# Kernel tuning notes

Hardware: AMD Instinct MI355X
Metric: run time of the kernel (lower is better)

## Reference

```python
import jax, jax.numpy as jnp
import numpy as np


def setup_inputs() -> dict:
    key = jax.random.key(0)
    k_x, k_w1, k_w2 = jax.random.split(key, 3)
    b, d, m, h = 256, 2048, 64, 128  # batch, d_model, history_length, d_out
    lim1 = 1.0 / np.sqrt(m + h)
    lim2 = 1.0 / np.sqrt(h + d)
    x = jax.random.normal(k_x, (b, d, m), dtype=jnp.float32)
    w1 = jax.random.uniform(k_w1, (m, h, d), dtype=jnp.float32, minval=-lim1, maxval=lim1)
    b1 = jnp.zeros((1, h, d), dtype=jnp.float32)
    w2 = jax.random.uniform(k_w2, (h, d), dtype=jnp.float32, minval=-lim2, maxval=lim2)
    b2 = jnp.zeros((1, h), dtype=jnp.float32)
    return {"x": x, "w1": w1, "b1": b1, "w2": w2, "b2": b2}


def reference(x, w1, b1, w2, b2):
    # per-neuron (per-d) MLP: contract over history m, then over hidden h
    hidden = jnp.einsum('bdm,mhd->bhd', x, w1) + b1  # (b, h, d)
    out = jnp.einsum('bhd,hd->bh', hidden, w2) + b2  # (b, h)
    return out
```

## Files before the change

### kernel.cpp

```cpp
#include <hip/hip_runtime.h>

typedef unsigned short u16;
typedef __attribute__((ext_vector_type(8))) short short8;
typedef __attribute__((ext_vector_type(4))) float f32x4;

#define D_TOT 2048
#define M_TOT 64
#define H_TOT 128
#define B_TOT 256
#define NG    256
#define XB    131072
#define W1M   262144

__device__ __forceinline__ u16 f2bf(float f) {
  unsigned u = __builtin_bit_cast(unsigned, f);
  u = (u + 0x7fffu + ((u >> 16) & 1u)) >> 16;
  return (u16)u;
}
__device__ __forceinline__ float bf2f(u16 v) {
  unsigned u = ((unsigned)v) << 16;
  return __builtin_bit_cast(float, u);
}

__global__ __launch_bounds__(256)
void nlm_p0(const float* __restrict__ b1, const float* __restrict__ w2,
            const float* __restrict__ b2, float* __restrict__ ch) {
  const int h = blockIdx.x, t = threadIdx.x;
  const float4* pb = (const float4*)(b1 + (size_t)h * D_TOT);
  const float4* pw = (const float4*)(w2 + (size_t)h * D_TOT);
  float s = 0.f;
  for (int i = t; i < D_TOT / 4; i += 256) {
    float4 a = pb[i], w = pw[i];
    s += a.x * w.x + a.y * w.y + a.z * w.z + a.w * w.w;
  }
  __shared__ float red[256];
  red[t] = s;
  __syncthreads();
  for (int off = 128; off > 0; off >>= 1) {
    if (t < off) red[t] += red[t + off];
    __syncthreads();
  }
  if (t == 0) ch[h] = red[0] + b2[h];
}

__global__ __launch_bounds__(256)
void nlm_pw(const float* __restrict__ w1, const float* __restrict__ w2,
            u16* __restrict__ Bp) {
  const int gq  = blockIdx.x & 63;
  const int hb  = blockIdx.x >> 6;
  const int dq0 = gq * 32;
  const int t   = threadIdx.x;
  __shared__ u16 tile[32 * 16 * 64];

#pragma unroll
  for (int rep = 0; rep < 4; ++rep) {
    const int tau = rep * 256 + t;
    const int h_l = tau >> 6, m = tau & 63;
    const int h   = hb * 16 + h_l;
    const float* w1p = w1 + (size_t)m * W1M + (size_t)h * D_TOT + dq0;
    const float* w2p = w2 + (size_t)h * D_TOT + dq0;
    u16* dst = tile + h_l * 64 + m;
#pragma unroll
    for (int q = 0; q < 8; ++q) {
      float4 a = *(const float4*)(w1p + q * 4);
      float4 s = *(const float4*)(w2p + q * 4);
      dst[(q * 4 + 0) * 1024] = f2bf(a.x * s.x);
      dst[(q * 4 + 1) * 1024] = f2bf(a.y * s.y);
      dst[(q * 4 + 2) * 1024] = f2bf(a.z * s.z);
      dst[(q * 4 + 3) * 1024] = f2bf(a.w * s.w);
    }
  }
  __syncthreads();
#pragma unroll 4
  for (int dc = 0; dc < 32; ++dc) {
    const int g = gq * 4 + (dc >> 3), c = dc & 7;
    u16* out = Bp + (((size_t)g * 8 + c) * H_TOT + hb * 16) * 64 + t * 4;
    *(ushort4*)out = *(const ushort4*)(tile + dc * 1024 + t * 4);
  }
}

__global__ __launch_bounds__(512, 4)
void nlm_p1(const float* __restrict__ x, const u16* __restrict__ Bp,
            u16* __restrict__ partial) {
  __shared__ __align__(16) u16 As[64 * 72];
  __shared__ __align__(16) u16 Bs[128 * 72];

  const int tid  = threadIdx.x;
  const int g    = blockIdx.x & 255;
  const int bq   = blockIdx.x >> 8;
  const int d0   = g * 8;
  const int lane = tid & 63, wave = tid >> 6;
  const int wm   = wave >> 2;
  const int wn   = wave & 3;
  const int quad = lane >> 4, l16 = lane & 15;

  const int a_bl = tid >> 3, a_p = tid & 7;
  const float* xrow = x + (size_t)(bq * 64 + a_bl) * XB
                        + (size_t)d0 * M_TOT + a_p * 8;
  const int b_h = tid >> 2, b_qp = tid & 3;
  const u16* bsrc = Bp + ((size_t)g * 8 * H_TOT + b_h) * 64 + b_qp * 16;

  f32x4 acc[2][2];
#pragma unroll
  for (int i = 0; i < 2; ++i)
#pragma unroll
    for (int j = 0; j < 2; ++j) acc[i][j] = (f32x4){0.f, 0.f, 0.f, 0.f};

  for (int c = 0; c < 8; ++c) {
    {
      const float* xp = xrow + c * M_TOT;
      float4 v0 = *(const float4*)(xp);
      float4 v1 = *(const float4*)(xp + 4);
      short8 av;
      av[0] = (short)f2bf(v0.x); av[1] = (short)f2bf(v0.y);
      av[2] = (short)f2bf(v0.z); av[3] = (short)f2bf(v0.w);
      av[4] = (short)f2bf(v1.x); av[5] = (short)f2bf(v1.y);
      av[6] = (short)f2bf(v1.z); av[7] = (short)f2bf(v1.w);
      *(short8*)(As + a_bl * 72 + a_p * 8) = av;
    }
    {
      const u16* bp = bsrc + (size_t)c * (H_TOT * 64);
      *(short8*)(Bs + b_h * 72 + b_qp * 16)     = *(const short8*)(bp);
      *(short8*)(Bs + b_h * 72 + b_qp * 16 + 8) = *(const short8*)(bp + 8);
    }
    __syncthreads();
#pragma unroll
    for (int s = 0; s < 2; ++s) {
      short8 af[2], bf[2];
#pragma unroll
      for (int i = 0; i < 2; ++i)
        af[i] = *(const short8*)(As + (wm * 32 + i * 16 + l16) * 72 + s * 32 + quad * 8);
#pragma unroll
      for (int j = 0; j < 2; ++j)
        bf[j] = *(const short8*)(Bs + (wn * 32 + j * 16 + l16) * 72 + s * 32 + quad * 8);
#pragma unroll
      for (int i = 0; i < 2; ++i)
#pragma unroll
        for (int j = 0; j < 2; ++j)
          acc[i][j] = __builtin_amdgcn_mfma_f32_16x16x32_bf16(af[i], bf[j], acc[i][j], 0, 0, 0);
    }
    __syncthreads();
  }

#pragma unroll
  for (int i = 0; i < 2; ++i)
#pragma unroll
    for (int j = 0; j < 2; ++j) {
      const int hcol = wn * 32 + j * 16 + l16;
#pragma unroll
      for (int r = 0; r < 4; ++r) {
        const int brow = bq * 64 + wm * 32 + i * 16 + quad * 4 + r;
        partial[((size_t)brow * NG + g) * H_TOT + hcol] = f2bf(acc[i][j][r]);
      }
    }
}

__global__ __launch_bounds__(256)
void nlm_p2(const u16* __restrict__ partial, const float* __restrict__ ch,
            float* __restrict__ out) {
  const int b = blockIdx.x, t = threadIdx.x;
  const int h2   = t & 63;
  const int half = t >> 6;
  const u16* base = partial + ((size_t)b * NG + half * 64) * H_TOT + 2 * h2;
  float s0 = 0.f, s1 = 0.f;
#pragma unroll 8
  for (int gg = 0; gg < 64; ++gg) {
    unsigned v = __builtin_nontemporal_load((const unsigned*)(base + (size_t)gg * H_TOT));
    s0 += bf2f((u16)(v & 0xffffu));
    s1 += bf2f((u16)(v >> 16));
  }
  __shared__ float red0[256], red1[256];
  red0[t] = s0;
  red1[t] = s1;
  __syncthreads();
  if (t < 64) {
    float a0 = red0[t] + red0[t + 64] + red0[t + 128] + red0[t + 192];
    float a1 = red1[t] + red1[t + 64] + red1[t + 128] + red1[t + 192];
    out[(size_t)b * H_TOT + 2 * t]     = a0 + ch[2 * t];
    out[(size_t)b * H_TOT + 2 * t + 1] = a1 + ch[2 * t + 1];
  }
}

extern "C" void kernel_launch(void* const* d_in, const int* in_sizes, int n_in,
                              void* d_out, int out_size, void* d_ws, size_t ws_size,
                              hipStream_t stream) {
  const float* x  = (const float*)d_in[0];
  const float* w1 = (const float*)d_in[1];
  const float* b1 = (const float*)d_in[2];
  const float* w2 = (const float*)d_in[3];
  const float* b2 = (const float*)d_in[4];
  float* out = (float*)d_out;

  u16*   partial = (u16*)d_ws;
  u16*   Bp      = (u16*)((char*)d_ws + (size_t)B_TOT * NG * H_TOT * sizeof(u16));
  float* ch      = (float*)((char*)d_ws + (size_t)B_TOT * NG * H_TOT * sizeof(u16)
                                        + (size_t)NG * 8 * H_TOT * 64 * sizeof(u16));

  nlm_p0<<<dim3(128),  dim3(256), 0, stream>>>(b1, w2, b2, ch);
  nlm_pw<<<dim3(512),  dim3(256), 0, stream>>>(w1, w2, Bp);
  nlm_p1<<<dim3(1024), dim3(512), 0, stream>>>(x, Bp, partial);
  nlm_p2<<<dim3(256),  dim3(256), 0, stream>>>(partial, ch, out);
}
```

Before: 267.7 us.

## Merge bias kernel into weight prep, halve prep tiles, prefetch next chunk in GEMM

Folds the bias-dot kernel into the weight-prep kernel as extra blocks, which removes one launch. The prep tiles are halved to 8 hidden rows, doubling the block count to 1024 plus 128 bias blocks. The main GEMM kernel now loads the x and B data for the next chunk into registers right after the barrier, so global loads overlap with the MFMA work, and the chunk loop is fully unrolled. This adds register pressure under launch bounds of 512 threads and 4 blocks, and the prep stores shrink to ushort2.

```diff
diff --git a/kernel.cpp b/kernel.cpp
--- a/kernel.cpp
+++ b/kernel.cpp
@@ -23,40 +23,41 @@
 }
 
 __global__ __launch_bounds__(256)
-void nlm_p0(const float* __restrict__ b1, const float* __restrict__ w2,
-            const float* __restrict__ b2, float* __restrict__ ch) {
-  const int h = blockIdx.x, t = threadIdx.x;
-  const float4* pb = (const float4*)(b1 + (size_t)h * D_TOT);
-  const float4* pw = (const float4*)(w2 + (size_t)h * D_TOT);
-  float s = 0.f;
-  for (int i = t; i < D_TOT / 4; i += 256) {
-    float4 a = pb[i], w = pw[i];
-    s += a.x * w.x + a.y * w.y + a.z * w.z + a.w * w.w;
-  }
-  __shared__ float red[256];
-  red[t] = s;
-  __syncthreads();
-  for (int off = 128; off > 0; off >>= 1) {
-    if (t < off) red[t] += red[t + off];
+void nlm_pw(const float* __restrict__ w1, const float* __restrict__ w2,
+            const float* __restrict__ b1, const float* __restrict__ b2,
+            u16* __restrict__ Bp, float* __restrict__ ch) {
+  __shared__ __align__(16) u16 tile[32 * 8 * 64];
+  const int t = threadIdx.x;
+
+  if (blockIdx.x >= 1024) {
+    const int h = blockIdx.x - 1024;
+    const float4* pb = (const float4*)(b1 + (size_t)h * D_TOT);
+    const float4* pw = (const float4*)(w2 + (size_t)h * D_TOT);
+    float s = 0.f;
+    for (int i = t; i < D_TOT / 4; i += 256) {
+      float4 a = pb[i], w = pw[i];
+      s += a.x * w.x + a.y * w.y + a.z * w.z + a.w * w.w;
+    }
+    float* red = (float*)tile;
+    red[t] = s;
     __syncthreads();
-  }
-  if (t == 0) ch[h] = red[0] + b2[h];
-}
-
-__global__ __launch_bounds__(256)
-void nlm_pw(const float* __restrict__ w1, const float* __restrict__ w2,
-            u16* __restrict__ Bp) {
+    for (int off = 128; off > 0; off >>= 1) {
+      if (t < off) red[t] += red[t + off];
+      __syncthreads();
+    }
+    if (t == 0) ch[h] = red[0] + b2[h];
+    return;
+  }
+
   const int gq  = blockIdx.x & 63;
   const int hb  = blockIdx.x >> 6;
   const int dq0 = gq * 32;
-  const int t   = threadIdx.x;
-  __shared__ u16 tile[32 * 16 * 64];
-
-#pragma unroll
-  for (int rep = 0; rep < 4; ++rep) {
+
+#pragma unroll
+  for (int rep = 0; rep < 2; ++rep) {
     const int tau = rep * 256 + t;
     const int h_l = tau >> 6, m = tau & 63;
-    const int h   = hb * 16 + h_l;
+    const int h   = hb * 8 + h_l;
     const float* w1p = w1 + (size_t)m * W1M + (size_t)h * D_TOT + dq0;
     const float* w2p = w2 + (size_t)h * D_TOT + dq0;
     u16* dst = tile + h_l * 64 + m;
@@ -64,18 +65,18 @@
     for (int q = 0; q < 8; ++q) {
       float4 a = *(const float4*)(w1p + q * 4);
       float4 s = *(const float4*)(w2p + q * 4);
-      dst[(q * 4 + 0) * 1024] = f2bf(a.x * s.x);
-      dst[(q * 4 + 1) * 1024] = f2bf(a.y * s.y);
-      dst[(q * 4 + 2) * 1024] = f2bf(a.z * s.z);
-      dst[(q * 4 + 3) * 1024] = f2bf(a.w * s.w);
+      dst[(q * 4 + 0) * 512] = f2bf(a.x * s.x);
+      dst[(q * 4 + 1) * 512] = f2bf(a.y * s.y);
+      dst[(q * 4 + 2) * 512] = f2bf(a.z * s.z);
+      dst[(q * 4 + 3) * 512] = f2bf(a.w * s.w);
     }
   }
   __syncthreads();
 #pragma unroll 4
   for (int dc = 0; dc < 32; ++dc) {
     const int g = gq * 4 + (dc >> 3), c = dc & 7;
-    u16* out = Bp + (((size_t)g * 8 + c) * H_TOT + hb * 16) * 64 + t * 4;
-    *(ushort4*)out = *(const ushort4*)(tile + dc * 1024 + t * 4);
+    u16* out = Bp + (((size_t)g * 8 + c) * H_TOT + hb * 8) * 64 + t * 2;
+    *(ushort2*)out = *(const ushort2*)(tile + dc * 512 + t * 2);
   }
 }
 
@@ -106,38 +107,46 @@
 #pragma unroll
     for (int j = 0; j < 2; ++j) acc[i][j] = (f32x4){0.f, 0.f, 0.f, 0.f};
 
+  float4 v0  = *(const float4*)(xrow);
+  float4 v1  = *(const float4*)(xrow + 4);
+  short8 bv0 = *(const short8*)(bsrc);
+  short8 bv1 = *(const short8*)(bsrc + 8);
+
+#pragma unroll
   for (int c = 0; c < 8; ++c) {
     {
-      const float* xp = xrow + c * M_TOT;
-      float4 v0 = *(const float4*)(xp);
-      float4 v1 = *(const float4*)(xp + 4);
       short8 av;
       av[0] = (short)f2bf(v0.x); av[1] = (short)f2bf(v0.y);
       av[2] = (short)f2bf(v0.z); av[3] = (short)f2bf(v0.w);
       av[4] = (short)f2bf(v1.x); av[5] = (short)f2bf(v1.y);
       av[6] = (short)f2bf(v1.z); av[7] = (short)f2bf(v1.w);
       *(short8*)(As + a_bl * 72 + a_p * 8) = av;
-    }
-    {
-      const u16* bp = bsrc + (size_t)c * (H_TOT * 64);
-      *(short8*)(Bs + b_h * 72 + b_qp * 16)     = *(const short8*)(bp);
-      *(short8*)(Bs + b_h * 72 + b_qp * 16 + 8) = *(const short8*)(bp + 8);
+      *(short8*)(Bs + b_h * 72 + b_qp * 16)     = bv0;
+      *(short8*)(Bs + b_h * 72 + b_qp * 16 + 8) = bv1;
     }
     __syncthreads();
+    if (c < 7) {
+      const float* xp = xrow + (c + 1) * M_TOT;
+      v0 = *(const float4*)(xp);
+      v1 = *(const float4*)(xp + 4);
+      const u16* bp = bsrc + (size_t)(c + 1) * (H_TOT * 64);
+      bv0 = *(const short8*)(bp);
+      bv1 = *(const short8*)(bp + 8);
+    }
 #pragma unroll
     for (int s = 0; s < 2; ++s) {
-      short8 af[2], bf[2];
+      short8 af[2], bfr[2];
 #pragma unroll
       for (int i = 0; i < 2; ++i)
         af[i] = *(const short8*)(As + (wm * 32 + i * 16 + l16) * 72 + s * 32 + quad * 8);
 #pragma unroll
       for (int j = 0; j < 2; ++j)
-        bf[j] = *(const short8*)(Bs + (wn * 32 + j * 16 + l16) * 72 + s * 32 + quad * 8);
+        bfr[j] = *(const short8*)(Bs + (wn * 32 + j * 16 + l16) * 72 + s * 32 + quad * 8);
 #pragma unroll
       for (int i = 0; i < 2; ++i)
 #pragma unroll
         for (int j = 0; j < 2; ++j)
-          acc[i][j] = __builtin_amdgcn_mfma_f32_16x16x32_bf16(af[i], bf[j], acc[i][j], 0, 0, 0);
+          acc[i][j] = __builtin_amdgcn_mfma_f32_16x16x32_bf16(af[i], bfr[j], acc[i][j], 0, 0, 0);
     }
     __syncthreads();
   }
@@ -196,8 +205,7 @@
   float* ch      = (float*)((char*)d_ws + (size_t)B_TOT * NG * H_TOT * sizeof(u16)
                                         + (size_t)NG * 8 * H_TOT * 64 * sizeof(u16));
 
-  nlm_p0<<<dim3(128),  dim3(256), 0, stream>>>(b1, w2, b2, ch);
-  nlm_pw<<<dim3(512),  dim3(256), 0, stream>>>(w1, w2, Bp);
+  nlm_pw<<<dim3(1152), dim3(256), 0, stream>>>(w1, w2, b1, b2, Bp, ch);
   nlm_p1<<<dim3(1024), dim3(512), 0, stream>>>(x, Bp, partial);
   nlm_p2<<<dim3(256),  dim3(256), 0, stream>>>(partial, ch, out);
 }
```

New measurement: 262.2 us. -2.1%, faster.

## Fuse weight prep into GEMM kernel with resident LDS weights and double-buffered x

Applied to the files above, without the earlier changes.

Merges the weight-scaling kernel into the main MFMA kernel: each block builds its w1*w2 bf16 slice (8 d-values, all h and m) once in LDS with an XOR swizzle. The block then loops over all four batch quarters, so the Bp global round-trip and one kernel launch go away. The x tile is prefetched two chunks ahead into registers and double-buffered in LDS, with one barrier per step instead of two. The cost is a 128KB LDS footprint and a grid of only 256 blocks, which lowers occupancy and parallelism.

```diff
diff --git a/kernel.cpp b/kernel.cpp
--- a/kernel.cpp
+++ b/kernel.cpp
@@ -43,116 +43,143 @@
   if (t == 0) ch[h] = red[0] + b2[h];
 }
 
-__global__ __launch_bounds__(256)
-void nlm_pw(const float* __restrict__ w1, const float* __restrict__ w2,
-            u16* __restrict__ Bp) {
-  const int gq  = blockIdx.x & 63;
-  const int hb  = blockIdx.x >> 6;
-  const int dq0 = gq * 32;
-  const int t   = threadIdx.x;
-  __shared__ u16 tile[32 * 16 * 64];
-
-#pragma unroll
-  for (int rep = 0; rep < 4; ++rep) {
-    const int tau = rep * 256 + t;
-    const int h_l = tau >> 6, m = tau & 63;
-    const int h   = hb * 16 + h_l;
-    const float* w1p = w1 + (size_t)m * W1M + (size_t)h * D_TOT + dq0;
-    const float* w2p = w2 + (size_t)h * D_TOT + dq0;
-    u16* dst = tile + h_l * 64 + m;
-#pragma unroll
-    for (int q = 0; q < 8; ++q) {
-      float4 a = *(const float4*)(w1p + q * 4);
-      float4 s = *(const float4*)(w2p + q * 4);
-      dst[(q * 4 + 0) * 1024] = f2bf(a.x * s.x);
-      dst[(q * 4 + 1) * 1024] = f2bf(a.y * s.y);
-      dst[(q * 4 + 2) * 1024] = f2bf(a.z * s.z);
-      dst[(q * 4 + 3) * 1024] = f2bf(a.w * s.w);
+__global__ __launch_bounds__(512, 2)
+void nlm_main(const float* __restrict__ x, const float* __restrict__ w1,
+              const float* __restrict__ w2, u16* __restrict__ partial) {
+  __shared__ __align__(16) u16 Bs[8 * H_TOT * 64];
+  __shared__ __align__(16) u16 As[2][64 * 72];
+
+  const int tid  = threadIdx.x;
+  const int lane = tid & 63, wave = tid >> 6;
+  const int g    = ((blockIdx.x & 7) << 5) + (blockIdx.x >> 3);
+  const int d0   = g * 8;
+
+  const int a_bl = tid >> 3, a_p = tid & 7;
+  const float* xbase = x + (size_t)a_bl * XB + (size_t)d0 * M_TOT + a_p * 8;
+
+  float4 e0 = *(const float4*)(xbase);
+  float4 e1 = *(const float4*)(xbase + 4);
+
+  {
+    const int m = lane;
+#pragma unroll 4
+    for (int rep = 0; rep < 16; ++rep) {
+      const int h = wave * 16 + rep;
+      const float* w1p = w1 + (size_t)m * W1M + (size_t)h * D_TOT + d0;
+      const float* w2p = w2 + (size_t)h * D_TOT + d0;
+      float4 a0 = *(const float4*)(w1p);
+      float4 a1 = *(const float4*)(w1p + 4);
+      float4 s0 = *(const float4*)(w2p);
+      float4 s1 = *(const float4*)(w2p + 4);
+      u16* dst = (u16*)((char*)Bs + h * 128 + ((m * 2) ^ ((h & 7) << 4)));
+      dst[0 * 8192] = f2bf(a0.x * s0.x);
+      dst[1 * 8192] = f2bf(a0.y * s0.y);
+      dst[2 * 8192] = f2bf(a0.z * s0.z);
+      dst[3 * 8192] = f2bf(a0.w * s0.w);
+      dst[4 * 8192] = f2bf(a1.x * s1.x);
+      dst[5 * 8192] = f2bf(a1.y * s1.y);
+      dst[6 * 8192] = f2bf(a1.z * s1.z);
+      dst[7 * 8192] = f2bf(a1.w * s1.w);
     }
   }
   __syncthreads();
-#pragma unroll 4
-  for (int dc = 0; dc < 32; ++dc) {
-    const int g = gq * 4 + (dc >> 3), c = dc & 7;
-    u16* out = Bp + (((size_t)g * 8 + c) * H_TOT + hb * 16) * 64 + t * 4;
-    *(ushort4*)out = *(const ushort4*)(tile + dc * 1024 + t * 4);
-  }
-}
-
-__global__ __launch_bounds__(512, 4)
-void nlm_p1(const float* __restrict__ x, const u16* __restrict__ Bp,
-            u16* __restrict__ partial) {
-  __shared__ __align__(16) u16 As[64 * 72];
-  __shared__ __align__(16) u16 Bs[128 * 72];
-
-  const int tid  = threadIdx.x;
-  const int g    = blockIdx.x & 255;
-  const int bq   = blockIdx.x >> 8;
-  const int d0   = g * 8;
-  const int lane = tid & 63, wave = tid >> 6;
-  const int wm   = wave >> 2;
-  const int wn   = wave & 3;
+
+  const int wm = wave >> 2, wn = wave & 3;
   const int quad = lane >> 4, l16 = lane & 15;
-
-  const int a_bl = tid >> 3, a_p = tid & 7;
-  const float* xrow = x + (size_t)(bq * 64 + a_bl) * XB
-                        + (size_t)d0 * M_TOT + a_p * 8;
-  const int b_h = tid >> 2, b_qp = tid & 3;
-  const u16* bsrc = Bp + ((size_t)g * 8 * H_TOT + b_h) * 64 + b_qp * 16;
+  const int q16 = quad * 16;
+
+  int aoff[2][2];
+#pragma unroll
+  for (int i = 0; i < 2; ++i)
+#pragma unroll
+    for (int s = 0; s < 2; ++s)
+      aoff[i][s] = (wm * 32 + i * 16 + l16) * 72 + s * 32 + quad * 8;
+
+  int boff[2][2];
+#pragma unroll
+  for (int j = 0; j < 2; ++j) {
+    const int hr = wn * 32 + j * 16 + l16;
+    const int bx = (hr & 7) << 4;
+#pragma unroll
+    for (int s = 0; s < 2; ++s)
+      boff[j][s] = hr * 128 + ((s * 64 + q16) ^ bx);
+  }
+
+  {
+    short8 av;
+    av[0] = (short)f2bf(e0.x); av[1] = (short)f2bf(e0.y);
+    av[2] = (short)f2bf(e0.z); av[3] = (short)f2bf(e0.w);
+    av[4] = (short)f2bf(e1.x); av[5] = (short)f2bf(e1.y);
+    av[6] = (short)f2bf(e1.z); av[7] = (short)f2bf(e1.w);
+    *(short8*)(&As[0][0] + a_bl * 72 + a_p * 8) = av;
+  }
+  float4 p00, p01, p10, p11;
+  {
+    const float* xp = xbase + 1 * M_TOT;
+    p10 = *(const float4*)(xp);
+    p11 = *(const float4*)(xp + 4);
+  }
+  asm volatile("s_waitcnt lgkmcnt(0)" ::: "memory");
+  __builtin_amdgcn_s_barrier();
 
   f32x4 acc[2][2];
-#pragma unroll
-  for (int i = 0; i < 2; ++i)
-#pragma unroll
-    for (int j = 0; j < 2; ++j) acc[i][j] = (f32x4){0.f, 0.f, 0.f, 0.f};
-
-  for (int c = 0; c < 8; ++c) {
-    {
-      const float* xp = xrow + c * M_TOT;
-      float4 v0 = *(const float4*)(xp);
-      float4 v1 = *(const float4*)(xp + 4);
-      short8 av;
-      av[0] = (short)f2bf(v0.x); av[1] = (short)f2bf(v0.y);
-      av[2] = (short)f2bf(v0.z); av[3] = (short)f2bf(v0.w);
-      av[4] = (short)f2bf(v1.x); av[5] = (short)f2bf(v1.y);
-      av[6] = (short)f2bf(v1.z); av[7] = (short)f2bf(v1.w);
-      *(short8*)(As + a_bl * 72 + a_p * 8) = av;
+
+  for (int bq = 0; bq < 4; ++bq) {
+#pragma unroll
+    for (int i = 0; i < 2; ++i)
+#pragma unroll
+      for (int j = 0; j < 2; ++j) acc[i][j] = (f32x4){0.f, 0.f, 0.f, 0.f};
+
+#pragma unroll
+    for (int c = 0; c < 8; ++c) {
+      if (bq < 3 || c < 6) {
+        const int bq2 = (c < 6) ? bq : bq + 1;
+        const int c2  = (c < 6) ? c + 2 : c - 6;
+        const float* xp = xbase + (size_t)bq2 * (64 * (size_t)XB) + c2 * M_TOT;
+        if ((c & 1) == 0) { p00 = *(const float4*)(xp); p01 = *(const float4*)(xp + 4); }
+        else              { p10 = *(const float4*)(xp); p11 = *(const float4*)(xp + 4); }
+      }
+      {
+        const u16*  Ab = &As[c & 1][0];
+        const char* Bb = (const char*)Bs + c * 16384;
+#pragma unroll
+        for (int s = 0; s < 2; ++s) {
+          short8 af0 = *(const short8*)(Ab + aoff[0][s]);
+          short8 af1 = *(const short8*)(Ab + aoff[1][s]);
+          short8 bf0 = *(const short8*)(Bb + boff[0][s]);
+          short8 bf1 = *(const short8*)(Bb + boff[1][s]);
+          acc[0][0] = __builtin_amdgcn_mfma_f32_16x16x32_bf16(af0, bf0, acc[0][0], 0, 0, 0);
+          acc[0][1] = __builtin_amdgcn_mfma_f32_16x16x32_bf16(af0, bf1, acc[0][1], 0, 0, 0);
+          acc[1][0] = __builtin_amdgcn_mfma_f32_16x16x32_bf16(af1, bf0, acc[1][0], 0, 0, 0);
+          acc[1][1] = __builtin_amdgcn_mfma_f32_16x16x32_bf16(af1, bf1, acc[1][1], 0, 0, 0);
+        }
+      }
+      if (bq < 3 || c < 7) {
+        float4 s0 = ((c + 1) & 1) ? p10 : p00;
+        float4 s1 = ((c + 1) & 1) ? p11 : p01;
+        short8 av;
+        av[0] = (short)f2bf(s0.x); av[1] = (short)f2bf(s0.y);
+        av[2] = (short)f2bf(s0.z); av[3] = (short)f2bf(s0.w);
+        av[4] = (short)f2bf(s1.x); av[5] = (short)f2bf(s1.y);
+        av[6] = (short)f2bf(s1.z); av[7] = (short)f2bf(s1.w);
+        *(short8*)(&As[(c + 1) & 1][0] + a_bl * 72 + a_p * 8) = av;
+      }
+      asm volatile("s_waitcnt lgkmcnt(0)" ::: "memory");
+      __builtin_amdgcn_s_barrier();
     }
-    {
-      const u16* bp = bsrc + (size_t)c * (H_TOT * 64);
-      *(short8*)(Bs + b_h * 72 + b_qp * 16)     = *(const short8*)(bp);
-      *(short8*)(Bs + b_h * 72 + b_qp * 16 + 8) = *(const short8*)(bp + 8);
-    }
-    __syncthreads();
-#pragma unroll
-    for (int s = 0; s < 2; ++s) {
-      short8 af[2], bf[2];
-#pragma unroll
-      for (int i = 0; i < 2; ++i)
-        af[i] = *(const short8*)(As + (wm * 32 + i * 16 + l16) * 72 + s * 32 + quad * 8);
-#pragma unroll
-      for (int j = 0; j < 2; ++j)
-        bf[j] = *(const short8*)(Bs + (wn * 32 + j * 16 + l16) * 72 + s * 32 + quad * 8);
-#pragma unroll
-      for (int i = 0; i < 2; ++i)
-#pragma unroll
-        for (int j = 0; j < 2; ++j)
-          acc[i][j] = __builtin_amdgcn_mfma_f32_16x16x32_bf16(af[i], bf[j], acc[i][j], 0, 0, 0);
-    }
-    __syncthreads();
-  }
-
-#pragma unroll
-  for (int i = 0; i < 2; ++i)
-#pragma unroll
-    for (int j = 0; j < 2; ++j) {
-      const int hcol = wn * 32 + j * 16 + l16;
-#pragma unroll
-      for (int r = 0; r < 4; ++r) {
-        const int brow = bq * 64 + wm * 32 + i * 16 + quad * 4 + r;
-        partial[((size_t)brow * NG + g) * H_TOT + hcol] = f2bf(acc[i][j][r]);
-      }
-    }
+
+#pragma unroll
+    for (int i = 0; i < 2; ++i)
+#pragma unroll
+      for (int j = 0; j < 2; ++j) {
+        const int hcol = wn * 32 + j * 16 + l16;
+#pragma unroll
+        for (int r = 0; r < 4; ++r) {
+          const int brow = bq * 64 + wm * 32 + i * 16 + quad * 4 + r;
+          partial[((size_t)brow * NG + g) * H_TOT + hcol] = f2bf(acc[i][j][r]);
+        }
+      }
+  }
 }
 
 __global__ __launch_bounds__(256)
@@ -192,12 +219,9 @@
   float* out = (float*)d_out;
 
   u16*   partial = (u16*)d_ws;
-  u16*   Bp      = (u16*)((char*)d_ws + (size_t)B_TOT * NG * H_TOT * sizeof(u16));
-  float* ch      = (float*)((char*)d_ws + (size_t)B_TOT * NG * H_TOT * sizeof(u16)
-                                        + (size_t)NG * 8 * H_TOT * 64 * sizeof(u16));
-
-  nlm_p0<<<dim3(128),  dim3(256), 0, stream>>>(b1, w2, b2, ch);
-  nlm_pw<<<dim3(512),  dim3(256), 0, stream>>>(w1, w2, Bp);
-  nlm_p1<<<dim3(1024), dim3(512), 0, stream>>>(x, Bp, partial);
-  nlm_p2<<<dim3(256),  dim3(256), 0, stream>>>(partial, ch, out);
-}
+  float* ch      = (float*)((char*)d_ws + (size_t)B_TOT * NG * H_TOT * sizeof(u16));
+
+  nlm_p0<<<dim3(128),   dim3(256), 0, stream>>>(b1, w2, b2, ch);
+  nlm_main<<<dim3(256), dim3(512), 0, stream>>>(x, w1, w2, partial);
+  nlm_p2<<<dim3(256),   dim3(256), 0, stream>>>(partial, ch, out);
+}
```

Result: no change. 266.3 us (-0.5%).
